# Kernel tuning notes

Measured on AMD Instinct MI355X. Metric: run time of the kernel, lower is better.

The kernel has to match this reference:

```python
import jax, jax.numpy as jnp
import numpy as np

HOPS = 3  # max_hops; C has HOPS+1 embedding tables


def setup_inputs() -> dict:
    key = jax.random.key(0)
    k1, k2 = jax.random.split(key)
    # story: [memory_len, batch, token_size]
    story = jax.random.randint(k1, (2048, 64, 4), 0, 50000, dtype=jnp.int64)
    # stacked embedding tables C_0..C_3: [hop+1, vocab, embed_dim], N(0, 0.1)
    C = 0.1 * jax.random.normal(k2, (HOPS + 1, 50000, 128), dtype=jnp.float32)
    return {"story": story, "C": C}


def reference(story, C):
    # story: [M, B, T] -> [B, M, T]
    story = jnp.transpose(story, (1, 0, 2))
    B, M, T = story.shape
    D = C.shape[-1]
    # padding_idx=0 semantics: embedding of token 0 is zero (fwd and bwd)
    pad_mask = (story != 0).astype(C.dtype)[..., None]  # [B, M, T, 1]

    u = jnp.zeros((B, D), dtype=C.dtype)
    for hop in range(HOPS):
        # gather + mask + sum over token dim -> memory keys m_A: [B, M, D]
        m_A = jnp.sum(C[hop][story] * pad_mask, axis=2)
        # attention scores over memory slots, softmax along M
        prob = jax.nn.softmax(jnp.einsum('bmd,bd->bm', m_A, u), axis=1)
        # memory values m_C from next-hop table: [B, M, D]
        m_C = jnp.sum(C[hop + 1][story] * pad_mask, axis=2)
        o_k = jnp.einsum('bm,bmd->bd', prob, m_C)
        u = u + o_k
    return u
```

## Files before the change

### kernel.cpp

```cpp
#include <hip/hip_runtime.h>

#define MM 2048
#define BB 64
#define TT 4
#define DD 128
#define VV 50000
#define VPAD 50176
#define NPART 392

typedef float f4v __attribute__((ext_vector_type(4)));
typedef short s8v __attribute__((ext_vector_type(8)));

__device__ __forceinline__ unsigned short f2bf(float f) {
    unsigned int u = __float_as_uint(f);
    u = u + 0x7FFFu + ((u >> 16) & 1u);
    return (unsigned short)(u >> 16);
}

__global__ void k_init(float4* __restrict__ p) {
    p[blockIdx.x * 256 + threadIdx.x] = make_float4(0.f, 0.f, 0.f, 0.f);
}

__global__ __launch_bounds__(256, 4) void k_gemm_p(const float* __restrict__ Ch,
                                                   const float* __restrict__ u,
                                                   float* __restrict__ P,
                                                   float* __restrict__ Z) {
    __shared__ short lds[128 * 136];
    const int t = threadIdx.x;
    const int v0 = blockIdx.x * 64;

    if (blockIdx.x == 0 && t < 64) Z[t] = 0.f;

#pragma unroll
    for (int i = 0; i < 16; ++i) {
        const int G = i * 256 + t;
        const int row = G >> 5;
        const int c4 = G & 31;
        float4 val;
        if (row < 64) {
            const int v = v0 + row;
            val = (v < VV) ? *(const float4*)(Ch + (size_t)v * DD + c4 * 4)
                           : make_float4(0.f, 0.f, 0.f, 0.f);
        } else {
            val = *(const float4*)(u + (size_t)(row - 64) * DD + c4 * 4);
        }
        const unsigned int lo = ((unsigned int)f2bf(val.y) << 16) | f2bf(val.x);
        const unsigned int hi = ((unsigned int)f2bf(val.w) << 16) | f2bf(val.z);
        *(uint2*)(lds + row * 136 + c4 * 4) = make_uint2(lo, hi);
    }
    __syncthreads();

    const int l = t & 63;
    const int w = t >> 6;
    const int quad = l >> 4;
    const int n16 = l & 15;

    const int arow = (16 * w + n16) * 136;
    const int brow0 = (64 + 0 * 16 + n16) * 136;
    const int brow1 = (64 + 1 * 16 + n16) * 136;
    const int brow2 = (64 + 2 * 16 + n16) * 136;
    const int brow3 = (64 + 3 * 16 + n16) * 136;

    f4v ac0 = {0.f, 0.f, 0.f, 0.f}, ac1 = ac0, ac2 = ac0, ac3 = ac0;

#pragma unroll
    for (int s = 0; s < 4; ++s) {
        const int ko = s * 32 + quad * 8;
        const s8v av = *(const s8v*)(lds + arow + ko);
        const s8v b0 = *(const s8v*)(lds + brow0 + ko);
        const s8v b1 = *(const s8v*)(lds + brow1 + ko);
        const s8v b2 = *(const s8v*)(lds + brow2 + ko);
        const s8v b3 = *(const s8v*)(lds + brow3 + ko);
        ac0 = __builtin_amdgcn_mfma_f32_16x16x32_bf16(av, b0, ac0, 0, 0, 0);
        ac1 = __builtin_amdgcn_mfma_f32_16x16x32_bf16(av, b1, ac1, 0, 0, 0);
        ac2 = __builtin_amdgcn_mfma_f32_16x16x32_bf16(av, b2, ac2, 0, 0, 0);
        ac3 = __builtin_amdgcn_mfma_f32_16x16x32_bf16(av, b3, ac3, 0, 0, 0);
    }

    const int vbase = v0 + 16 * w + quad * 4;
#pragma unroll
    for (int r = 0; r < 4; ++r) {
        float* __restrict__ Pr = P + (size_t)(vbase + r) * 64 + n16;
        Pr[0]  = ac0[r];
        Pr[16] = ac1[r];
        Pr[32] = ac2[r];
        Pr[48] = ac3[r];
    }
}

__global__ __launch_bounds__(256) void k_attn2(const int* __restrict__ st,
                                               const float* __restrict__ P,
                                               float* __restrict__ W,
                                               float* __restrict__ Z) {
    __shared__ float eb[256];
    const int tid = threadIdx.x;
    const int g = blockIdx.x * 256 + tid;
    const int b = g & 63;

    const int4 tk = *(const int4*)(st + (size_t)g * 4);
    float s = 0.f;
    if (tk.x) s += P[(size_t)tk.x * 64 + b];
    if (tk.y) s += P[(size_t)tk.y * 64 + b];
    if (tk.z) s += P[(size_t)tk.z * 64 + b];
    if (tk.w) s += P[(size_t)tk.w * 64 + b];
    const float e = __expf(s);
    eb[tid] = e;

    if (tk.x) atomicAdd(W + (size_t)tk.x * 64 + b, e);
    if (tk.y) atomicAdd(W + (size_t)tk.y * 64 + b, e);
    if (tk.z) atomicAdd(W + (size_t)tk.z * 64 + b, e);
    if (tk.w) atomicAdd(W + (size_t)tk.w * 64 + b, e);

    __syncthreads();
    if (tid < 64)
        atomicAdd(Z + tid, (eb[tid] + eb[tid + 64]) + (eb[tid + 128] + eb[tid + 192]));
}

__global__ __launch_bounds__(256, 3) void k_gemm_o(const float* __restrict__ C2,
                                                   float* __restrict__ W,
                                                   float* __restrict__ upart,
                                                   const int rezero) {
    __shared__ float Wl[64 * 68];
    __shared__ float Cl[64 * 136];
    const int t = threadIdx.x;
    const int g = t >> 7;
    const int b0 = ((t >> 4) & 7) * 8;
    const int d0 = (t & 15) * 8;
    const int vb = blockIdx.x * 128;

    f4v a0l = {0.f, 0.f, 0.f, 0.f}, a0h = a0l, a1l = a0l, a1h = a0l;
    f4v a2l = a0l, a2h = a0l, a3l = a0l, a3h = a0l;
    f4v a4l = a0l, a4h = a0l, a5l = a0l, a5h = a0l;
    f4v a6l = a0l, a6h = a0l, a7l = a0l, a7h = a0l;

    for (int cc = 0; cc < 2; ++cc) {
        const int vc = vb + cc * 64;
#pragma unroll
        for (int i = 0; i < 4; ++i) {
            const int G = i * 256 + t;
            const int row = G >> 4, c4 = G & 15;
            float* wp = W + (size_t)(vc + row) * 64 + c4 * 4;
            const float4 val = *(const float4*)wp;
            *(float4*)&Wl[row * 68 + c4 * 4] = val;
            if (rezero) *(float4*)wp = make_float4(0.f, 0.f, 0.f, 0.f);
        }
#pragma unroll
        for (int i = 0; i < 8; ++i) {
            const int G = i * 256 + t;
            const int row = G >> 5, c4 = G & 31;
            const int v = vc + row;
            float4 val = (v < VV) ? *(const float4*)(C2 + (size_t)v * DD + c4 * 4)
                                  : make_float4(0.f, 0.f, 0.f, 0.f);
            *(float4*)&Cl[row * 136 + c4 * 4] = val;
        }
        __syncthreads();

#define FMA_ROW(al, ah, wc)            \
    al += wc * cA; ah += wc * cB;

#pragma unroll
        for (int j = 0; j < 32; ++j) {
            const int kk = g * 32 + j;
            const f4v wA = *(const f4v*)&Wl[kk * 68 + b0];
            const f4v wB = *(const f4v*)&Wl[kk * 68 + b0 + 4];
            const f4v cA = *(const f4v*)&Cl[kk * 136 + d0];
            const f4v cB = *(const f4v*)&Cl[kk * 136 + d0 + 4];
            FMA_ROW(a0l, a0h, wA[0]) FMA_ROW(a1l, a1h, wA[1])
            FMA_ROW(a2l, a2h, wA[2]) FMA_ROW(a3l, a3h, wA[3])
            FMA_ROW(a4l, a4h, wB[0]) FMA_ROW(a5l, a5h, wB[1])
            FMA_ROW(a6l, a6h, wB[2]) FMA_ROW(a7l, a7h, wB[3])
        }
#undef FMA_ROW
        __syncthreads();
    }

    if (g == 1) {
#define STL(i, al, ah)                                   \
        *(f4v*)&Cl[(b0 + i) * 136 + d0] = al;            \
        *(f4v*)&Cl[(b0 + i) * 136 + d0 + 4] = ah;
        STL(0, a0l, a0h) STL(1, a1l, a1h) STL(2, a2l, a2h) STL(3, a3l, a3h)
        STL(4, a4l, a4h) STL(5, a5l, a5h) STL(6, a6l, a6h) STL(7, a7l, a7h)
#undef STL
    }
    __syncthreads();
    if (g == 0) {
        float* __restrict__ up = upart + (size_t)blockIdx.x * (BB * DD);
#define STG(i, al, ah) {                                             \
        const f4v xl = al + *(const f4v*)&Cl[(b0 + i) * 136 + d0];   \
        const f4v xh = ah + *(const f4v*)&Cl[(b0 + i) * 136 + d0 + 4]; \
        *(f4v*)(up + (b0 + i) * DD + d0) = xl;                       \
        *(f4v*)(up + (b0 + i) * DD + d0 + 4) = xh; }
        STG(0, a0l, a0h) STG(1, a1l, a1h) STG(2, a2l, a2h) STG(3, a3l, a3h)
        STG(4, a4l, a4h) STG(5, a5l, a5h) STG(6, a6l, a6h) STG(7, a7l, a7h)
#undef STG
    }
}

__global__ __launch_bounds__(256) void k_reduce_u(const float* __restrict__ up,
                                                  const float* __restrict__ Z,
                                                  float* __restrict__ u) {
    const int jc = blockIdx.x & 31;
    const int kc = blockIdx.x >> 5;
    const int j = jc * 256 + threadIdx.x;
    const float* __restrict__ p = up + (size_t)kc * 49 * (BB * DD) + j;
    float s = 0.f;
#pragma unroll 7
    for (int k = 0; k < 49; ++k) s += p[(size_t)k * (BB * DD)];
    const float rz = 1.f / Z[j >> 7];
    atomicAdd(u + j, s * rz);
}

__global__ void k_copy(const float* __restrict__ u, float* __restrict__ out) {
    const int i = blockIdx.x * 256 + threadIdx.x;
    out[i] = u[i];
}

extern "C" void kernel_launch(void* const* d_in, const int* in_sizes, int n_in,
                              void* d_out, int out_size, void* d_ws, size_t ws_size,
                              hipStream_t stream) {
    const int* st = (const int*)d_in[0];
    const float* C = (const float*)d_in[1];

    float* u  = (float*)d_ws;
    float* W  = u + BB * DD;
    float* P  = W + (size_t)VPAD * BB;
    float* up = P + (size_t)VPAD * BB;
    float* Z  = up + (size_t)NPART * BB * DD;

    k_init<<<(BB * DD + VPAD * BB) / 1024, 256, 0, stream>>>((float4*)u);

    for (int hop = 0; hop < 3; ++hop) {
        const float* Ch  = C + (size_t)hop * VV * DD;
        const float* Ch1 = C + (size_t)(hop + 1) * VV * DD;

        k_gemm_p<<<VPAD / 64, 256, 0, stream>>>(Ch, u, P, Z);
        k_attn2<<<(MM * BB) / 256, 256, 0, stream>>>(st, P, W, Z);
        k_gemm_o<<<VPAD / 128, 256, 0, stream>>>(Ch1, W, up,
                                                 hop < 2 ? 1 : 0);
        k_reduce_u<<<256, 256, 0, stream>>>(up, Z, u);
    }

    k_copy<<<(BB * DD) / 256, 256, 0, stream>>>(u, (float*)d_out);
}
```

Baseline: 383.7 us.

## Fuse all hops into one persistent kernel with software grid barriers

Replaces the per-hop chain of launches with a single persistent kernel of 512 blocks that moves between phases through atomic-counter grid barriers. It also skips the hop-0 score GEMM because u starts at zero, giving uniform weights, and computes the softmax per batch row inside one block instead of using a global Z accumulator. The P GEMM tile is enlarged to 128 rows per block, and the partial-sum reduction becomes a single pass over all partials. The aim is to remove launch gaps and the first-hop GEMM, but the barriers depend on all blocks being co-resident, the reductions now run on only a few blocks, and the spin loop has a timeout that breaks out without synchronising.

```diff
diff --git a/kernel.cpp b/kernel.cpp
--- a/kernel.cpp
+++ b/kernel.cpp
@@ -7,6 +7,8 @@
 #define VV 50000
 #define VPAD 50176
 #define NPART 392
+#define NBLK 512
+#define NBAR 16
 
 typedef float f4v __attribute__((ext_vector_type(4)));
 typedef short s8v __attribute__((ext_vector_type(8)));
@@ -17,32 +19,53 @@
     return (unsigned short)(u >> 16);
 }
 
-__global__ void k_init(float4* __restrict__ p) {
-    p[blockIdx.x * 256 + threadIdx.x] = make_float4(0.f, 0.f, 0.f, 0.f);
-}
-
-__global__ __launch_bounds__(256, 4) void k_gemm_p(const float* __restrict__ Ch,
-                                                   const float* __restrict__ u,
-                                                   float* __restrict__ P,
-                                                   float* __restrict__ Z) {
-    __shared__ short lds[128 * 136];
-    const int t = threadIdx.x;
-    const int v0 = blockIdx.x * 64;
-
-    if (blockIdx.x == 0 && t < 64) Z[t] = 0.f;
-
-#pragma unroll
-    for (int i = 0; i < 16; ++i) {
+union LdsU {
+    short gp[192 * 136];
+    struct { float Wl[64 * 68]; float Cl[64 * 136]; } go;
+    float red[64];
+};
+
+__global__ void k_binit(float4* __restrict__ p, unsigned* __restrict__ bar) {
+    const int i = blockIdx.x * 256 + threadIdx.x;
+    p[i] = make_float4(0.f, 0.f, 0.f, 0.f);
+    if (i < NBAR) bar[i] = 0u;
+}
+
+__device__ __forceinline__ void gbar(unsigned* __restrict__ bar, int idx) {
+    __syncthreads();
+    if (threadIdx.x == 0) {
+        __threadfence();
+        unsigned* c = bar + idx;
+        atomicAdd(c, 1u);
+        int polls = 0;
+        while (__hip_atomic_load(c, __ATOMIC_RELAXED,
+                                 __HIP_MEMORY_SCOPE_AGENT) < (unsigned)NBLK) {
+            __builtin_amdgcn_s_sleep(2);
+            if (++polls > (1 << 18)) break;
+        }
+        __threadfence();
+    }
+    __syncthreads();
+}
+
+__device__ __forceinline__ void gemm_p128(LdsU& L, int tile, int t,
+                                          const float* __restrict__ Ch,
+                                          const float* __restrict__ u,
+                                          float* __restrict__ P) {
+    short* lds = L.gp;
+    const int v0 = tile * 128;
+#pragma unroll
+    for (int i = 0; i < 24; ++i) {
         const int G = i * 256 + t;
         const int row = G >> 5;
         const int c4 = G & 31;
         float4 val;
-        if (row < 64) {
+        if (row < 128) {
             const int v = v0 + row;
             val = (v < VV) ? *(const float4*)(Ch + (size_t)v * DD + c4 * 4)
                            : make_float4(0.f, 0.f, 0.f, 0.f);
         } else {
-            val = *(const float4*)(u + (size_t)(row - 64) * DD + c4 * 4);
+            val = *(const float4*)(u + (size_t)(row - 128) * DD + c4 * 4);
         }
         const unsigned int lo = ((unsigned int)f2bf(val.y) << 16) | f2bf(val.x);
         const unsigned int hi = ((unsigned int)f2bf(val.w) << 16) | f2bf(val.z);
@@ -55,78 +78,92 @@
     const int quad = l >> 4;
     const int n16 = l & 15;
 
-    const int arow = (16 * w + n16) * 136;
-    const int brow0 = (64 + 0 * 16 + n16) * 136;
-    const int brow1 = (64 + 1 * 16 + n16) * 136;
-    const int brow2 = (64 + 2 * 16 + n16) * 136;
-    const int brow3 = (64 + 3 * 16 + n16) * 136;
-
-    f4v ac0 = {0.f, 0.f, 0.f, 0.f}, ac1 = ac0, ac2 = ac0, ac3 = ac0;
+    const int ar0 = (32 * w + n16) * 136;
+    const int ar1 = (32 * w + 16 + n16) * 136;
+    const int br0 = (128 + n16) * 136;
+    const int br1 = (144 + n16) * 136;
+    const int br2 = (160 + n16) * 136;
+    const int br3 = (176 + n16) * 136;
+
+    f4v c00 = {0.f, 0.f, 0.f, 0.f}, c01 = c00, c02 = c00, c03 = c00;
+    f4v c10 = c00, c11 = c00, c12 = c00, c13 = c00;
 
 #pragma unroll
     for (int s = 0; s < 4; ++s) {
         const int ko = s * 32 + quad * 8;
-        const s8v av = *(const s8v*)(lds + arow + ko);
-        const s8v b0 = *(const s8v*)(lds + brow0 + ko);
-        const s8v b1 = *(const s8v*)(lds + brow1 + ko);
-        const s8v b2 = *(const s8v*)(lds + brow2 + ko);
-        const s8v b3 = *(const s8v*)(lds + brow3 + ko);
-        ac0 = __builtin_amdgcn_mfma_f32_16x16x32_bf16(av, b0, ac0, 0, 0, 0);
-        ac1 = __builtin_amdgcn_mfma_f32_16x16x32_bf16(av, b1, ac1, 0, 0, 0);
-        ac2 = __builtin_amdgcn_mfma_f32_16x16x32_bf16(av, b2, ac2, 0, 0, 0);
-        ac3 = __builtin_amdgcn_mfma_f32_16x16x32_bf16(av, b3, ac3, 0, 0, 0);
-    }
-
-    const int vbase = v0 + 16 * w + quad * 4;
+        const s8v a0 = *(const s8v*)(lds + ar0 + ko);
+        const s8v a1 = *(const s8v*)(lds + ar1 + ko);
+        const s8v b0 = *(const s8v*)(lds + br0 + ko);
+        const s8v b1 = *(const s8v*)(lds + br1 + ko);
+        const s8v b2 = *(const s8v*)(lds + br2 + ko);
+        const s8v b3 = *(const s8v*)(lds + br3 + ko);
+        c00 = __builtin_amdgcn_mfma_f32_16x16x32_bf16(a0, b0, c00, 0, 0, 0);
+        c01 = __builtin_amdgcn_mfma_f32_16x16x32_bf16(a0, b1, c01, 0, 0, 0);
+        c02 = __builtin_amdgcn_mfma_f32_16x16x32_bf16(a0, b2, c02, 0, 0, 0);
+        c03 = __builtin_amdgcn_mfma_f32_16x16x32_bf16(a0, b3, c03, 0, 0, 0);
+        c10 = __builtin_amdgcn_mfma_f32_16x16x32_bf16(a1, b0, c10, 0, 0, 0);
+        c11 = __builtin_amdgcn_mfma_f32_16x16x32_bf16(a1, b1, c11, 0, 0, 0);
+        c12 = __builtin_amdgcn_mfma_f32_16x16x32_bf16(a1, b2, c12, 0, 0, 0);
+        c13 = __builtin_amdgcn_mfma_f32_16x16x32_bf16(a1, b3, c13, 0, 0, 0);
+    }
+
+    const int vb0 = v0 + 32 * w + quad * 4;
+    const int vb1 = vb0 + 16;
 #pragma unroll
     for (int r = 0; r < 4; ++r) {
-        float* __restrict__ Pr = P + (size_t)(vbase + r) * 64 + n16;
-        Pr[0]  = ac0[r];
-        Pr[16] = ac1[r];
-        Pr[32] = ac2[r];
-        Pr[48] = ac3[r];
-    }
-}
-
-__global__ __launch_bounds__(256) void k_attn2(const int* __restrict__ st,
-                                               const float* __restrict__ P,
-                                               float* __restrict__ W,
-                                               float* __restrict__ Z) {
-    __shared__ float eb[256];
-    const int tid = threadIdx.x;
-    const int g = blockIdx.x * 256 + tid;
-    const int b = g & 63;
-
-    const int4 tk = *(const int4*)(st + (size_t)g * 4);
-    float s = 0.f;
-    if (tk.x) s += P[(size_t)tk.x * 64 + b];
-    if (tk.y) s += P[(size_t)tk.y * 64 + b];
-    if (tk.z) s += P[(size_t)tk.z * 64 + b];
-    if (tk.w) s += P[(size_t)tk.w * 64 + b];
-    const float e = __expf(s);
-    eb[tid] = e;
-
-    if (tk.x) atomicAdd(W + (size_t)tk.x * 64 + b, e);
-    if (tk.y) atomicAdd(W + (size_t)tk.y * 64 + b, e);
-    if (tk.z) atomicAdd(W + (size_t)tk.z * 64 + b, e);
-    if (tk.w) atomicAdd(W + (size_t)tk.w * 64 + b, e);
-
-    __syncthreads();
-    if (tid < 64)
-        atomicAdd(Z + tid, (eb[tid] + eb[tid + 64]) + (eb[tid + 128] + eb[tid + 192]));
-}
-
-__global__ __launch_bounds__(256, 3) void k_gemm_o(const float* __restrict__ C2,
-                                                   float* __restrict__ W,
-                                                   float* __restrict__ upart,
-                                                   const int rezero) {
-    __shared__ float Wl[64 * 68];
-    __shared__ float Cl[64 * 136];
-    const int t = threadIdx.x;
+        float* __restrict__ P0 = P + (size_t)(vb0 + r) * 64 + n16;
+        P0[0] = c00[r]; P0[16] = c01[r]; P0[32] = c02[r]; P0[48] = c03[r];
+        float* __restrict__ P1 = P + (size_t)(vb1 + r) * 64 + n16;
+        P1[0] = c10[r]; P1[16] = c11[r]; P1[32] = c12[r]; P1[48] = c13[r];
+    }
+}
+
+__device__ __forceinline__ void attn256(LdsU& L, int b, int t,
+                                        const int* __restrict__ st,
+                                        const float* __restrict__ P,
+                                        float* __restrict__ W) {
+    int4 tk[8];
+    float e[8];
+#pragma unroll
+    for (int k = 0; k < 8; ++k)
+        tk[k] = *(const int4*)(st + ((size_t)(t + 256 * k) * 64 + b) * 4);
+#pragma unroll
+    for (int k = 0; k < 8; ++k) {
+        float s = 0.f;
+        if (tk[k].x) s += P[(size_t)tk[k].x * 64 + b];
+        if (tk[k].y) s += P[(size_t)tk[k].y * 64 + b];
+        if (tk[k].z) s += P[(size_t)tk[k].z * 64 + b];
+        if (tk[k].w) s += P[(size_t)tk[k].w * 64 + b];
+        e[k] = __expf(s);
+    }
+    float sum = ((e[0] + e[1]) + (e[2] + e[3])) + ((e[4] + e[5]) + (e[6] + e[7]));
+#pragma unroll
+    for (int off = 32; off; off >>= 1) sum += __shfl_xor(sum, off, 64);
+    if ((t & 63) == 0) L.red[t >> 6] = sum;
+    __syncthreads();
+    const float inv = 1.f / ((L.red[0] + L.red[1]) + (L.red[2] + L.red[3]));
+#pragma unroll
+    for (int k = 0; k < 8; ++k) {
+        const float p = e[k] * inv;
+        if (tk[k].x) atomicAdd(W + (size_t)tk[k].x * 64 + b, p);
+        if (tk[k].y) atomicAdd(W + (size_t)tk[k].y * 64 + b, p);
+        if (tk[k].z) atomicAdd(W + (size_t)tk[k].z * 64 + b, p);
+        if (tk[k].w) atomicAdd(W + (size_t)tk[k].w * 64 + b, p);
+    }
+    __syncthreads();
+}
+
+__device__ __forceinline__ void gemm_o_tile(LdsU& L, int tile, int t,
+                                            const float* __restrict__ C2,
+                                            float* __restrict__ W,
+                                            float* __restrict__ upart,
+                                            const int rezero) {
+    float* Wl = L.go.Wl;
+    float* Cl = L.go.Cl;
     const int g = t >> 7;
     const int b0 = ((t >> 4) & 7) * 8;
     const int d0 = (t & 15) * 8;
-    const int vb = blockIdx.x * 128;
+    const int vb = tile * 128;
 
     f4v a0l = {0.f, 0.f, 0.f, 0.f}, a0h = a0l, a1l = a0l, a1h = a0l;
     f4v a2l = a0l, a2h = a0l, a3l = a0l, a3h = a0l;
@@ -157,7 +194,6 @@
 
 #define FMA_ROW(al, ah, wc)            \
     al += wc * cA; ah += wc * cB;
-
 #pragma unroll
         for (int j = 0; j < 32; ++j) {
             const int kk = g * 32 + j;
@@ -184,7 +220,7 @@
     }
     __syncthreads();
     if (g == 0) {
-        float* __restrict__ up = upart + (size_t)blockIdx.x * (BB * DD);
+        float* __restrict__ up = upart + (size_t)tile * (BB * DD);
 #define STG(i, al, ah) {                                             \
         const f4v xl = al + *(const f4v*)&Cl[(b0 + i) * 136 + d0];   \
         const f4v xh = ah + *(const f4v*)&Cl[(b0 + i) * 136 + d0 + 4]; \
@@ -194,25 +230,65 @@
         STG(4, a4l, a4h) STG(5, a5l, a5h) STG(6, a6l, a6h) STG(7, a7l, a7h)
 #undef STG
     }
-}
-
-__global__ __launch_bounds__(256) void k_reduce_u(const float* __restrict__ up,
-                                                  const float* __restrict__ Z,
-                                                  float* __restrict__ u) {
-    const int jc = blockIdx.x & 31;
-    const int kc = blockIdx.x >> 5;
-    const int j = jc * 256 + threadIdx.x;
-    const float* __restrict__ p = up + (size_t)kc * 49 * (BB * DD) + j;
+    __syncthreads();
+}
+
+__device__ __forceinline__ void reduce_unit(int unit, int t,
+                                            const float* __restrict__ up,
+                                            const float* __restrict__ u,
+                                            float* __restrict__ dst) {
+    const int j = unit * 256 + t;
+    const float* __restrict__ p = up + j;
     float s = 0.f;
-#pragma unroll 7
-    for (int k = 0; k < 49; ++k) s += p[(size_t)k * (BB * DD)];
-    const float rz = 1.f / Z[j >> 7];
-    atomicAdd(u + j, s * rz);
-}
-
-__global__ void k_copy(const float* __restrict__ u, float* __restrict__ out) {
-    const int i = blockIdx.x * 256 + threadIdx.x;
-    out[i] = u[i];
+#pragma unroll 8
+    for (int k = 0; k < NPART; ++k) s += p[(size_t)k * (BB * DD)];
+    dst[j] = u[j] + s;
+}
+
+__global__ __launch_bounds__(256, 2) void k_mega(const int* __restrict__ st,
+                                                 const float* __restrict__ C,
+                                                 float* __restrict__ u,
+                                                 float* __restrict__ W,
+                                                 float* __restrict__ P,
+                                                 float* __restrict__ up,
+                                                 unsigned* __restrict__ bar,
+                                                 float* __restrict__ out) {
+    __shared__ LdsU L;
+    const int bid = blockIdx.x;
+    const int t = threadIdx.x;
+
+    {
+        const int g = bid * 256 + t;
+        const int b = g & 63;
+        const float p = 1.0f / (float)MM;
+        const int4 tk = *(const int4*)(st + (size_t)g * 4);
+        if (tk.x) atomicAdd(W + (size_t)tk.x * 64 + b, p);
+        if (tk.y) atomicAdd(W + (size_t)tk.y * 64 + b, p);
+        if (tk.z) atomicAdd(W + (size_t)tk.z * 64 + b, p);
+        if (tk.w) atomicAdd(W + (size_t)tk.w * 64 + b, p);
+    }
+    gbar(bar, 0);
+    if (bid < NPART) gemm_o_tile(L, bid, t, C + (size_t)1 * VV * DD, W, up, 1);
+    gbar(bar, 1);
+    if (bid < 32) reduce_unit(bid, t, up, u, u);
+    gbar(bar, 2);
+
+    if (bid < NPART) gemm_p128(L, bid, t, C + (size_t)1 * VV * DD, u, P);
+    gbar(bar, 3);
+    if (bid < BB) attn256(L, bid, t, st, P, W);
+    gbar(bar, 4);
+    if (bid < NPART) gemm_o_tile(L, bid, t, C + (size_t)2 * VV * DD, W, up, 1);
+    gbar(bar, 5);
+    if (bid < 32) reduce_unit(bid, t, up, u, u);
+    gbar(bar, 6);
+
+    if (bid < NPART) gemm_p128(L, bid, t, C + (size_t)2 * VV * DD, u, P);
+    gbar(bar, 7);
+    if (bid < BB) attn256(L, bid, t, st, P, W);
+    gbar(bar, 8);
+    if (bid < NPART) gemm_o_tile(L, bid, t, C + (size_t)3 * VV * DD, W, up, 0);
+    gbar(bar, 9);
+    if (bid < 32) reduce_unit(bid, t, up, u, out);
 }
 
 extern "C" void kernel_launch(void* const* d_in, const int* in_sizes, int n_in,
@@ -225,20 +301,9 @@
     float* W  = u + BB * DD;
     float* P  = W + (size_t)VPAD * BB;
     float* up = P + (size_t)VPAD * BB;
-    float* Z  = up + (size_t)NPART * BB * DD;
-
-    k_init<<<(BB * DD + VPAD * BB) / 1024, 256, 0, stream>>>((float4*)u);
-
-    for (int hop = 0; hop < 3; ++hop) {
-        const float* Ch  = C + (size_t)hop * VV * DD;
-        const float* Ch1 = C + (size_t)(hop + 1) * VV * DD;
-
-        k_gemm_p<<<VPAD / 64, 256, 0, stream>>>(Ch, u, P, Z);
-        k_attn2<<<(MM * BB) / 256, 256, 0, stream>>>(st, P, W, Z);
-        k_gemm_o<<<VPAD / 128, 256, 0, stream>>>(Ch1, W, up,
-                                                 hop < 2 ? 1 : 0);
-        k_reduce_u<<<256, 256, 0, stream>>>(up, Z, u);
-    }
-
-    k_copy<<<(BB * DD) / 256, 256, 0, stream>>>(u, (float*)d_out);
-}
+    unsigned* bar = (unsigned*)(up + (size_t)NPART * BB * DD);
+
+    k_binit<<<(BB * DD + VPAD * BB) / 1024, 256, 0, stream>>>((float4*)u, bar);
+
+    k_mega<<<NBLK, 256, 0, stream>>>(st, C, u, W, P, up, bar, (float*)d_out);
+}
```

Measured after the change: 867.0 us. 126% more time.
